# Optimization experiments

Measured on AMD Instinct MI355X. Metric: run time of the kernel, lower is better.

## Reference

```python
import jax, jax.numpy as jnp
import numpy as np

N_NODES = 50000
N_EDGES = 800000
N_GRAPHS = 512
HEADS = 4
HDIM = 64
NEG_SLOPE = 0.2


def setup_inputs() -> dict:
    key = jax.random.key(0)
    ks = jax.random.split(key, 16)
    x = jax.random.normal(ks[0], (N_NODES, 128), dtype=jnp.float32)
    edge_index = jax.random.randint(ks[1], (2, N_EDGES), 0, N_NODES, dtype=jnp.int64)
    batch = jnp.sort(jax.random.randint(ks[2], (N_NODES,), 0, N_GRAPHS, dtype=jnp.int64))
    def glorot(k, shape):
        fan = shape[0] + shape[-1]
        return jax.random.normal(k, shape, dtype=jnp.float32) * jnp.sqrt(2.0 / fan)
    return {
        "x": x, "edge_index": edge_index, "batch": batch,
        "W1": glorot(ks[3], (128, 256)), "a_src1": glorot(ks[4], (HEADS, HDIM)), "a_dst1": glorot(ks[5], (HEADS, HDIM)), "b1": jnp.zeros((256,), jnp.float32),
        "W2": glorot(ks[6], (256, 256)), "a_src2": glorot(ks[7], (HEADS, HDIM)), "a_dst2": glorot(ks[8], (HEADS, HDIM)), "b2": jnp.zeros((256,), jnp.float32),
        "W3": glorot(ks[9], (256, 256)), "a_src3": glorot(ks[10], (HEADS, HDIM)), "a_dst3": glorot(ks[11], (HEADS, HDIM)), "b3": jnp.zeros((256,), jnp.float32),
        "fc_W": glorot(ks[12], (256, 1)), "fc_b": jnp.zeros((1,), jnp.float32),
    }


def gat_layer(x, W, a_src, a_dst, b, src, dst):
    # x: [N, F_in] -> h: [N, H, C]
    N = x.shape[0]
    h = (x @ W).reshape(N, HEADS, HDIM)
    alpha_s = jnp.sum(h * a_src[None], axis=-1)  # [N, H]
    alpha_d = jnp.sum(h * a_dst[None], axis=-1)  # [N, H]
    logits = jax.nn.leaky_relu(alpha_s[src] + alpha_d[dst], NEG_SLOPE)  # [E, H]
    # segment softmax over destination nodes
    m = jax.ops.segment_max(logits, dst, num_segments=N)  # [N, H]
    e = jnp.exp(logits - m[dst])
    denom = jax.ops.segment_sum(e, dst, num_segments=N)
    alpha = e / denom[dst]  # [E, H]
    msg = h[src] * alpha[:, :, None]  # [E, H, C]
    out = jax.ops.segment_sum(msg, dst, num_segments=N).reshape(N, HEADS * HDIM)
    return out + b


def reference(x, edge_index, batch, W1, a_src1, a_dst1, b1, W2, a_src2, a_dst2, b2, W3, a_src3, a_dst3, b3, fc_W, fc_b):
    N = x.shape[0]
    loop = jnp.arange(N, dtype=edge_index.dtype)
    # PyG GATConv adds self-loops by default
    src = jnp.concatenate([edge_index[0], loop])
    dst = jnp.concatenate([edge_index[1], loop])
    h = gat_layer(x, W1, a_src1, a_dst1, b1, src, dst)
    h = gat_layer(h, W2, a_src2, a_dst2, b2, src, dst)
    h = gat_layer(h, W3, a_src3, a_dst3, b3, src, dst)
    pooled = jax.ops.segment_sum(h, batch, num_segments=N_GRAPHS)  # [G, 256]
    return pooled @ fc_W + fc_b
```

## Files before the change

### kernel.cpp

```cpp
#include <hip/hip_runtime.h>
#include <hip/hip_bf16.h>
#include <math.h>

#define NN 50000
#define NE 800000
#define ET (NE + NN)
#define EP (ET + 24)
#define NG 512
#define NEG 0.2f

typedef __attribute__((ext_vector_type(8))) short bf16x8;
typedef __attribute__((ext_vector_type(4))) float f32x4;

__device__ inline unsigned f2o(float f) {
    unsigned b = __float_as_uint(f);
    return (b & 0x80000000u) ? ~b : (b | 0x80000000u);
}
__device__ inline float o2f(unsigned u) {
    return (u & 0x80000000u) ? __uint_as_float(u ^ 0x80000000u) : __uint_as_float(~u);
}
__device__ inline unsigned short f2b(float f) {
    unsigned u = __float_as_uint(f);
    u += 0x7fffu + ((u >> 16) & 1u);
    return (unsigned short)(u >> 16);
}
__device__ inline float b2f(unsigned short b) {
    return __uint_as_float(((unsigned)b) << 16);
}

__global__ __launch_bounds__(256) void split_weights(const float* __restrict__ W1,
        const float* __restrict__ W2, const float* __restrict__ W3,
        unsigned short* __restrict__ WTh, unsigned short* __restrict__ WTl) {
    int tid = blockIdx.x * 256 + threadIdx.x;
    const float* W; int K, n, k, base;
    if (tid < 32768)       { W = W1; K = 128; base = 0;     int i = tid;          n = i >> 7; k = i & 127; }
    else if (tid < 98304)  { W = W2; K = 256; base = 32768; int i = tid - 32768;  n = i >> 8; k = i & 255; }
    else if (tid < 163840) { W = W3; K = 256; base = 98304; int i = tid - 98304;  n = i >> 8; k = i & 255; }
    else return;
    float w = W[k * 256 + n];
    unsigned short hi = f2b(w);
    float lo = w - b2f(hi);
    WTh[base + n * K + k] = hi;
    WTl[base + n * K + k] = f2b(lo);
}

template<int K, int AFP32>
__global__ __launch_bounds__(256) void gemm_mfma(const float* __restrict__ Af,
        const unsigned short* __restrict__ Ahi, const unsigned short* __restrict__ Alo,
        const unsigned short* __restrict__ Bhi, const unsigned short* __restrict__ Blo,
        unsigned short* __restrict__ h,
        const float* __restrict__ a_src, const float* __restrict__ a_dst,
        float* __restrict__ as_, float* __restrict__ ad_,
        unsigned* __restrict__ gmax) {
    __shared__ unsigned short AsH[128][40], AsL[128][40], BsH[128][40], BsL[128][40];
    const int t = threadIdx.x;
    const int mb = blockIdx.x >> 1, nb = blockIdx.x & 1;
    const int m0 = mb * 128, n0 = nb * 128;
    const int wid = t >> 6, lane = t & 63;
    const int wr = wid >> 1, wc = wid & 1;
    const int lr = lane & 15, lg = lane >> 4;

    f32x4 acc[4][4];
    #pragma unroll
    for (int mi = 0; mi < 4; ++mi)
        #pragma unroll
        for (int ni = 0; ni < 4; ++ni)
            acc[mi][ni] = (f32x4){0.f, 0.f, 0.f, 0.f};

    for (int k0 = 0; k0 < K; k0 += 32) {
        __syncthreads();
        #pragma unroll
        for (int cc = 0; cc < 2; ++cc) {
            int c = t + cc * 256;
            int row = c >> 2, kc = c & 3;
            int gr = m0 + row; if (gr >= NN) gr = NN - 1;
            if (AFP32) {
                const float* pa = Af + (size_t)gr * K + k0 + kc * 8;
                float4 f0 = *(const float4*)pa;
                float4 f1 = *(const float4*)(pa + 4);
                union { unsigned short u[8]; uint4 v; } th, tl;
                float fs[8] = {f0.x, f0.y, f0.z, f0.w, f1.x, f1.y, f1.z, f1.w};
                #pragma unroll
                for (int j = 0; j < 8; ++j) {
                    unsigned short hv = f2b(fs[j]);
                    th.u[j] = hv;
                    tl.u[j] = f2b(fs[j] - b2f(hv));
                }
                *(uint4*)&AsH[row][kc * 8] = th.v;
                *(uint4*)&AsL[row][kc * 8] = tl.v;
            } else {
                *(uint4*)&AsH[row][kc * 8] = *(const uint4*)(Ahi + (size_t)gr * K + k0 + kc * 8);
                *(uint4*)&AsL[row][kc * 8] = *(const uint4*)(Alo + (size_t)gr * K + k0 + kc * 8);
            }
            *(uint4*)&BsH[row][kc * 8] = *(const uint4*)(Bhi + (size_t)(n0 + row) * K + k0 + kc * 8);
            *(uint4*)&BsL[row][kc * 8] = *(const uint4*)(Blo + (size_t)(n0 + row) * K + k0 + kc * 8);
        }
        __syncthreads();

        bf16x8 ah[4], al[4];
        #pragma unroll
        for (int mi = 0; mi < 4; ++mi) {
            int ra = wr * 64 + mi * 16 + lr;
            ah[mi] = *(const bf16x8*)&AsH[ra][lg * 8];
            al[mi] = *(const bf16x8*)&AsL[ra][lg * 8];
        }
        #pragma unroll
        for (int ni = 0; ni < 4; ++ni) {
            int rb = wc * 64 + ni * 16 + lr;
            bf16x8 bh = *(const bf16x8*)&BsH[rb][lg * 8];
            bf16x8 bl = *(const bf16x8*)&BsL[rb][lg * 8];
            #pragma unroll
            for (int mi = 0; mi < 4; ++mi) {
                acc[mi][ni] = __builtin_amdgcn_mfma_f32_16x16x32_bf16(bh, ah[mi], acc[mi][ni], 0, 0, 0);
                acc[mi][ni] = __builtin_amdgcn_mfma_f32_16x16x32_bf16(bh, al[mi], acc[mi][ni], 0, 0, 0);
                acc[mi][ni] = __builtin_amdgcn_mfma_f32_16x16x32_bf16(bl, ah[mi], acc[mi][ni], 0, 0, 0);
            }
        }
    }

    const int head = nb * 2 + wc;
    const int ncol0 = n0 + wc * 64;
    float4 asv[4], adv[4];
    #pragma unroll
    for (int ni = 0; ni < 4; ++ni) {
        asv[ni] = *(const float4*)&a_src[head * 64 + ni * 16 + lg * 4];
        adv[ni] = *(const float4*)&a_dst[head * 64 + ni * 16 + lg * 4];
    }
    float pmax = -1e30f;
    #pragma unroll
    for (int mi = 0; mi < 4; ++mi) {
        float ps = 0.f, pd = 0.f;
        #pragma unroll
        for (int ni = 0; ni < 4; ++ni) {
            ps = fmaf(acc[mi][ni][0], asv[ni].x, ps); pd = fmaf(acc[mi][ni][0], adv[ni].x, pd);
            ps = fmaf(acc[mi][ni][1], asv[ni].y, ps); pd = fmaf(acc[mi][ni][1], adv[ni].y, pd);
            ps = fmaf(acc[mi][ni][2], asv[ni].z, ps); pd = fmaf(acc[mi][ni][2], adv[ni].z, pd);
            ps = fmaf(acc[mi][ni][3], asv[ni].w, ps); pd = fmaf(acc[mi][ni][3], adv[ni].w, pd);
        }
        ps += __shfl_xor(ps, 16, 64); ps += __shfl_xor(ps, 32, 64);
        pd += __shfl_xor(pd, 16, 64); pd += __shfl_xor(pd, 32, 64);
        pmax = fmaxf(pmax, ps);
        int row = m0 + wr * 64 + mi * 16 + lr;
        if (row < NN) {
            #pragma unroll
            for (int ni = 0; ni < 4; ++ni) {
                ushort4 hv = {f2b(acc[mi][ni][0]), f2b(acc[mi][ni][1]),
                              f2b(acc[mi][ni][2]), f2b(acc[mi][ni][3])};
                *(ushort4*)&h[(size_t)row * 256 + ncol0 + ni * 16 + lg * 4] = hv;
            }
            if (lane < 16) { as_[row * 4 + head] = ps; ad_[row * 4 + head] = pd; }
        }
    }
    pmax = fmaxf(pmax, __shfl_xor(pmax, 1, 64));
    pmax = fmaxf(pmax, __shfl_xor(pmax, 2, 64));
    pmax = fmaxf(pmax, __shfl_xor(pmax, 4, 64));
    pmax = fmaxf(pmax, __shfl_xor(pmax, 8, 64));
    if (lane == 0) atomicMax(&gmax[head], f2o(pmax));
}

__global__ void init_counts(int* counts, int* esrc_pad, int* edst_pad, unsigned* gmax) {
    int i = blockIdx.x * 256 + threadIdx.x;
    if (i < NN) counts[i] = 1;
    if (i < 24) { esrc_pad[i] = 0; edst_pad[i] = 0; }
    if (i < 12) gmax[i] = 0u;
}
__global__ void count_kernel(const int* __restrict__ dst, int* counts) {
    int e = blockIdx.x * 256 + threadIdx.x;
    if (e < NE) atomicAdd(&counts[dst[e]], 1);
}
__global__ __launch_bounds__(1024) void scan_kernel(const int* __restrict__ counts,
                                                    int* row_ptr, int* cursor) {
    __shared__ int sm[1024];
    const int i = threadIdx.x;
    const int CH = (NN + 1023) / 1024;
    int base = i * CH;
    int s = 0;
    for (int j = 0; j < CH; ++j) { int idx = base + j; if (idx < NN) s += counts[idx]; }
    sm[i] = s; __syncthreads();
    for (int off = 1; off < 1024; off <<= 1) {
        int v = (i >= off) ? sm[i - off] : 0;
        __syncthreads();
        sm[i] += v;
        __syncthreads();
    }
    int run = sm[i] - s;
    for (int j = 0; j < CH; ++j) {
        int idx = base + j;
        if (idx < NN) { row_ptr[idx] = run; cursor[idx] = run; run += counts[idx]; }
    }
    if (i == 1023) row_ptr[NN] = ET;
}
__global__ void scatter_kernel(const int* __restrict__ src, const int* __restrict__ dst,
                               int* cursor, int* esrc, int* edst) {
    int e = blockIdx.x * 256 + threadIdx.x;
    if (e < NE) {
        int d = dst[e];
        int p = atomicAdd(&cursor[d], 1);
        esrc[p] = src[e];
        edst[p] = d;
    } else if (e < ET) {
        int n = e - NE;
        int p = atomicAdd(&cursor[n], 1);
        esrc[p] = n;
        edst[p] = n;
    }
}

__global__ __launch_bounds__(256) void edge_w(const int* __restrict__ esrc,
        const int* __restrict__ edst, const float* __restrict__ aS,
        const float* __restrict__ aD, const unsigned* __restrict__ gmax,
        float* __restrict__ wE) {
    int idx = blockIdx.x * 256 + threadIdx.x;
    if (idx >= EP * 4) return;
    int e = idx >> 2, hd = idx & 3;
    if (e >= ET) { wE[idx] = 0.f; return; }
    int s = esrc[e], d = edst[e];
    float adn = aD[d * 4 + hd];
    float t = aS[s * 4 + hd] + adn; t = t > 0.f ? t : NEG * t;
    float g = o2f(gmax[hd]) + adn;  g = g > 0.f ? g : NEG * g;
    wE[idx] = __expf(t - g);
}

#define EDGE(we, he)                                                           \
    {                                                                          \
        lsum += (we);                                                          \
        acc.x = fmaf((we), b2f((he).x), acc.x);                                \
        acc.y = fmaf((we), b2f((he).y), acc.y);                                \
        acc.z = fmaf((we), b2f((he).z), acc.z);                                \
        acc.w = fmaf((we), b2f((he).w), acc.w);                                \
    }

template<int FINAL>
__global__ __launch_bounds__(256) void agg_kernel(const unsigned short* __restrict__ h,
        const float* __restrict__ wE,
        const int* __restrict__ row_ptr, const int* __restrict__ esrc,
        const float* __restrict__ bias,
        unsigned short* __restrict__ ohi, unsigned short* __restrict__ olo,
        float* __restrict__ out,
        const int* __restrict__ batch, const float* __restrict__ fcW) {
    int n = blockIdx.x * 4 + (threadIdx.x >> 6);
    int lane = threadIdx.x & 63;
    if (n >= NN) return;
    const int head = lane >> 4;
    const int c4 = lane * 4;
    int s0 = row_ptr[n], s1 = row_ptr[n + 1];
    float lsum = 0.f;
    float4 acc = {0.f, 0.f, 0.f, 0.f};

    int i = s0;
    int iA[4], iB[4];
    float wA[4]; ushort4 hA[4];
    #pragma unroll
    for (int j = 0; j < 4; ++j) iA[j] = esrc[i + j];
    #pragma unroll
    for (int j = 0; j < 4; ++j) iB[j] = esrc[i + 4 + j];
    #pragma unroll
    for (int j = 0; j < 4; ++j) wA[j] = wE[(i + j) * 4 + head];
    #pragma unroll
    for (int j = 0; j < 4; ++j) hA[j] = *(const ushort4*)&h[(long)iA[j] * 256 + c4];

    while (i + 8 <= s1) {
        int iC[4];
        #pragma unroll
        for (int j = 0; j < 4; ++j) iC[j] = esrc[i + 8 + j];
        float wB[4]; ushort4 hB[4];
        #pragma unroll
        for (int j = 0; j < 4; ++j) wB[j] = wE[(i + 4 + j) * 4 + head];
        #pragma unroll
        for (int j = 0; j < 4; ++j) hB[j] = *(const ushort4*)&h[(long)iB[j] * 256 + c4];
        #pragma unroll
        for (int j = 0; j < 4; ++j) EDGE(wA[j], hA[j]);
        #pragma unroll
        for (int j = 0; j < 4; ++j) { iB[j] = iC[j]; wA[j] = wB[j]; hA[j] = hB[j]; }
        i += 4;
    }
    if (i + 4 <= s1) {
        #pragma unroll
        for (int j = 0; j < 4; ++j) EDGE(wA[j], hA[j]);
        i += 4;
    }
    for (; i < s1; ++i) {
        float w = wE[i * 4 + head];
        ushort4 hv = *(const ushort4*)&h[(long)esrc[i] * 256 + c4];
        EDGE(w, hv);
    }

    float rl = 1.f / lsum;
    float4 bv = *(const float4*)&bias[c4];
    float4 o = {fmaf(acc.x, rl, bv.x), fmaf(acc.y, rl, bv.y),
                fmaf(acc.z, rl, bv.z), fmaf(acc.w, rl, bv.w)};
    if (!FINAL) {
        ushort4 vh = {f2b(o.x), f2b(o.y), f2b(o.z), f2b(o.w)};
        ushort4 vl = {f2b(o.x - b2f(vh.x)), f2b(o.y - b2f(vh.y)),
                      f2b(o.z - b2f(vh.z)), f2b(o.w - b2f(vh.w))};
        *(ushort4*)&ohi[(long)n * 256 + c4] = vh;
        *(ushort4*)&olo[(long)n * 256 + c4] = vl;
    } else {
        float4 fw = *(const float4*)&fcW[c4];
        float sd = o.x * fw.x + o.y * fw.y + o.z * fw.z + o.w * fw.w;
        #pragma unroll
        for (int off = 32; off; off >>= 1) sd += __shfl_xor(sd, off, 64);
        if (lane == 0) atomicAdd(&out[batch[n]], sd);
    }
}

__global__ void out_init(const float* __restrict__ fc_b, float* out) {
    int i = blockIdx.x * 256 + threadIdx.x;
    if (i < NG) out[i] = fc_b[0];
}

extern "C" void kernel_launch(void* const* d_in, const int* in_sizes, int n_in,
                              void* d_out, int out_size, void* d_ws, size_t ws_size,
                              hipStream_t stream) {
    const float* x      = (const float*)d_in[0];
    const int*   ei     = (const int*)d_in[1];
    const int*   batch  = (const int*)d_in[2];
    const float* W1     = (const float*)d_in[3];
    const float* as1    = (const float*)d_in[4];
    const float* ad1    = (const float*)d_in[5];
    const float* b1     = (const float*)d_in[6];
    const float* W2     = (const float*)d_in[7];
    const float* as2    = (const float*)d_in[8];
    const float* ad2    = (const float*)d_in[9];
    const float* b2     = (const float*)d_in[10];
    const float* W3     = (const float*)d_in[11];
    const float* as3    = (const float*)d_in[12];
    const float* ad3    = (const float*)d_in[13];
    const float* b3     = (const float*)d_in[14];
    const float* fcW    = (const float*)d_in[15];
    const float* fcb    = (const float*)d_in[16];
    const int* esrc_in = ei;
    const int* edst_in = ei + NE;

    char* ws = (char*)d_ws;
    size_t off = 0;
    unsigned short* hB  = (unsigned short*)(ws + off); off += (size_t)NN * 256 * 2;
    unsigned short* ohi = (unsigned short*)(ws + off); off += (size_t)NN * 256 * 2;
    unsigned short* olo = (unsigned short*)(ws + off); off += (size_t)NN * 256 * 2;
    unsigned short* WTh = (unsigned short*)(ws + off); off += 163840 * 2;
    unsigned short* WTl = (unsigned short*)(ws + off); off += 163840 * 2;
    float* aS    = (float*)(ws + off); off += (size_t)NN * 4 * 4;
    float* aD    = (float*)(ws + off); off += (size_t)NN * 4 * 4;
    int* counts  = (int*)(ws + off);   off += (size_t)NN * 4;
    int* cursor  = (int*)(ws + off);   off += (size_t)NN * 4;
    int* row_ptr = (int*)(ws + off);   off += (size_t)(NN + 1) * 4 + 12;
    unsigned* gmax = (unsigned*)(ws + off); off += 48;
    int* esrc    = (int*)(ws + off);   off += (size_t)EP * 4;
    int* edst    = (int*)(ws + off);   off += (size_t)EP * 4;
    float* wE    = (float*)(ws + off); off += (size_t)EP * 4 * 4;
    float* out   = (float*)d_out;

    init_counts<<<(NN + 255) / 256, 256, 0, stream>>>(counts, esrc + ET, edst + ET, gmax);
    count_kernel<<<(NE + 255) / 256, 256, 0, stream>>>(edst_in, counts);
    scan_kernel<<<1, 1024, 0, stream>>>(counts, row_ptr, cursor);
    scatter_kernel<<<(ET + 255) / 256, 256, 0, stream>>>(esrc_in, edst_in, cursor, esrc, edst);
    split_weights<<<640, 256, 0, stream>>>(W1, W2, W3, WTh, WTl);

    const int GEMM_GRID = ((NN + 127) / 128) * 2;
    const int NODE_GRID = (NN + 3) / 4;
    const int EW_GRID   = (EP * 4 + 255) / 256;

    gemm_mfma<128, 1><<<GEMM_GRID, 256, 0, stream>>>(x, nullptr, nullptr, WTh, WTl, hB, as1, ad1, aS, aD, gmax);
    edge_w<<<EW_GRID, 256, 0, stream>>>(esrc, edst, aS, aD, gmax, wE);
    agg_kernel<0><<<NODE_GRID, 256, 0, stream>>>(hB, wE, row_ptr, esrc, b1, ohi, olo, nullptr, nullptr, nullptr);
    gemm_mfma<256, 0><<<GEMM_GRID, 256, 0, stream>>>(nullptr, ohi, olo, WTh + 32768, WTl + 32768, hB, as2, ad2, aS, aD, gmax + 4);
    edge_w<<<EW_GRID, 256, 0, stream>>>(esrc, edst, aS, aD, gmax + 4, wE);
    agg_kernel<0><<<NODE_GRID, 256, 0, stream>>>(hB, wE, row_ptr, esrc, b2, ohi, olo, nullptr, nullptr, nullptr);
    gemm_mfma<256, 0><<<GEMM_GRID, 256, 0, stream>>>(nullptr, ohi, olo, WTh + 98304, WTl + 98304, hB, as3, ad3, aS, aD, gmax + 8);
    edge_w<<<EW_GRID, 256, 0, stream>>>(esrc, edst, aS, aD, gmax + 8, wE);
    out_init<<<(NG + 255) / 256, 256, 0, stream>>>(fcb, out);
    agg_kernel<1><<<NODE_GRID, 256, 0, stream>>>(hB, wE, row_ptr, esrc, b3, nullptr, nullptr, out, batch, fcW);
}
```

Baseline: 681.2 us.

## Stage neighbor feature rows into LDS via global_load_lds in aggregation

Rewrites the aggregation inner loop to gather eight neighbor feature rows per iteration directly into shared memory using global_load_lds, then read them back from LDS for the weighted accumulation. This replaces the previous register software pipeline with a batched load plus full vmcnt wait, and pads edge arrays further so eight-wide index prefetch stays in bounds. The intent is to issue more gathers in flight per wave, at the cost of adding an LDS round trip and a full wait that serializes load and compute within each batch.

After: 745.1 us. 9.4% more time.

```diff
diff --git a/kernel.cpp b/kernel.cpp
--- a/kernel.cpp
+++ b/kernel.cpp
@@ -5,12 +5,18 @@
 #define NN 50000
 #define NE 800000
 #define ET (NE + NN)
-#define EP (ET + 24)
+#define EP (ET + 40)
 #define NG 512
 #define NEG 0.2f
 
 typedef __attribute__((ext_vector_type(8))) short bf16x8;
 typedef __attribute__((ext_vector_type(4))) float f32x4;
+typedef __attribute__((address_space(1))) const unsigned int g_u32;
+typedef __attribute__((address_space(3))) unsigned int l_u32;
+
+__device__ __forceinline__ void gload4(const void* g, void* l) {
+    __builtin_amdgcn_global_load_lds((g_u32*)g, (l_u32*)l, 4, 0, 0);
+}
 
 __device__ inline unsigned f2o(float f) {
     unsigned b = __float_as_uint(f);
@@ -161,7 +167,7 @@
 __global__ void init_counts(int* counts, int* esrc_pad, int* edst_pad, unsigned* gmax) {
     int i = blockIdx.x * 256 + threadIdx.x;
     if (i < NN) counts[i] = 1;
-    if (i < 24) { esrc_pad[i] = 0; edst_pad[i] = 0; }
+    if (i < 40) { esrc_pad[i] = 0; edst_pad[i] = 0; }
     if (i < 12) gmax[i] = 0u;
 }
 __global__ void count_kernel(const int* __restrict__ dst, int* counts) {
@@ -221,15 +227,6 @@
     wE[idx] = __expf(t - g);
 }
 
-#define EDGE(we, he)                                                           \
-    {                                                                          \
-        lsum += (we);                                                          \
-        acc.x = fmaf((we), b2f((he).x), acc.x);                                \
-        acc.y = fmaf((we), b2f((he).y), acc.y);                                \
-        acc.z = fmaf((we), b2f((he).z), acc.z);                                \
-        acc.w = fmaf((we), b2f((he).w), acc.w);                                \
-    }
-
 template<int FINAL>
 __global__ __launch_bounds__(256) void agg_kernel(const unsigned short* __restrict__ h,
         const float* __restrict__ wE,
@@ -238,8 +235,10 @@
         unsigned short* __restrict__ ohi, unsigned short* __restrict__ olo,
         float* __restrict__ out,
         const int* __restrict__ batch, const float* __restrict__ fcW) {
-    int n = blockIdx.x * 4 + (threadIdx.x >> 6);
-    int lane = threadIdx.x & 63;
+    __shared__ unsigned int stage[4][8][128];
+    const int wid = threadIdx.x >> 6;
+    const int lane = threadIdx.x & 63;
+    int n = blockIdx.x * 4 + wid;
     if (n >= NN) return;
     const int head = lane >> 4;
     const int c4 = lane * 4;
@@ -247,42 +246,44 @@
     float lsum = 0.f;
     float4 acc = {0.f, 0.f, 0.f, 0.f};
 
+    int idx[8];
+    #pragma unroll
+    for (int j = 0; j < 8; ++j) idx[j] = esrc[s0 + j];
+
     int i = s0;
-    int iA[4], iB[4];
-    float wA[4]; ushort4 hA[4];
-    #pragma unroll
-    for (int j = 0; j < 4; ++j) iA[j] = esrc[i + j];
-    #pragma unroll
-    for (int j = 0; j < 4; ++j) iB[j] = esrc[i + 4 + j];
-    #pragma unroll
-    for (int j = 0; j < 4; ++j) wA[j] = wE[(i + j) * 4 + head];
-    #pragma unroll
-    for (int j = 0; j < 4; ++j) hA[j] = *(const ushort4*)&h[(long)iA[j] * 256 + c4];
-
-    while (i + 8 <= s1) {
-        int iC[4];
-        #pragma unroll
-        for (int j = 0; j < 4; ++j) iC[j] = esrc[i + 8 + j];
-        float wB[4]; ushort4 hB[4];
-        #pragma unroll
-        for (int j = 0; j < 4; ++j) wB[j] = wE[(i + 4 + j) * 4 + head];
-        #pragma unroll
-        for (int j = 0; j < 4; ++j) hB[j] = *(const ushort4*)&h[(long)iB[j] * 256 + c4];
-        #pragma unroll
-        for (int j = 0; j < 4; ++j) EDGE(wA[j], hA[j]);
-        #pragma unroll
-        for (int j = 0; j < 4; ++j) { iB[j] = iC[j]; wA[j] = wB[j]; hA[j] = hB[j]; }
-        i += 4;
-    }
-    if (i + 4 <= s1) {
-        #pragma unroll
-        for (int j = 0; j < 4; ++j) EDGE(wA[j], hA[j]);
-        i += 4;
-    }
-    for (; i < s1; ++i) {
-        float w = wE[i * 4 + head];
-        ushort4 hv = *(const ushort4*)&h[(long)esrc[i] * 256 + c4];
-        EDGE(w, hv);
+    while (i < s1) {
+        int valid = s1 - i;
+        #pragma unroll
+        for (int j4 = 0; j4 < 8; j4 += 4) {
+            if (j4 < valid) {
+                #pragma unroll
+                for (int j = j4; j < j4 + 4; ++j) {
+                    const char* row = (const char*)(h + (size_t)idx[j] * 256);
+                    gload4(row + lane * 8,     &stage[wid][j][0]);
+                    gload4(row + lane * 8 + 4, &stage[wid][j][64]);
+                }
+            }
+        }
+        int nidx[8];
+        #pragma unroll
+        for (int j = 0; j < 8; ++j) nidx[j] = esrc[i + 8 + j];
+        asm volatile("s_waitcnt vmcnt(0)" ::: "memory");
+        __builtin_amdgcn_sched_barrier(0);
+        #pragma unroll
+        for (int j = 0; j < 8; ++j) {
+            float wraw = wE[(size_t)(i + j) * 4 + head];
+            float w = (j < valid) ? wraw : 0.f;
+            lsum += w;
+            unsigned u0 = stage[wid][j][lane];
+            unsigned u1 = stage[wid][j][64 + lane];
+            acc.x = fmaf(w, __uint_as_float(u0 << 16), acc.x);
+            acc.y = fmaf(w, __uint_as_float(u0 & 0xffff0000u), acc.y);
+            acc.z = fmaf(w, __uint_as_float(u1 << 16), acc.z);
+            acc.w = fmaf(w, __uint_as_float(u1 & 0xffff0000u), acc.w);
+        }
+        #pragma unroll
+        for (int j = 0; j < 8; ++j) idx[j] = nidx[j];
+        i += 8;
     }
 
     float rl = 1.f / lsum;
```
